# Kernel tuning notes

Measured on AMD Instinct MI355X. Metric: run time of the kernel, lower is better.

Reference implementation:

```python
import jax, jax.numpy as jnp
import numpy as np

B, F, K, DEPTH = 512, 64, 64, 3  # feas == k == 64, deepDepth == 3


def setup_inputs() -> dict:
    key = jax.random.key(0)
    ks = jax.random.split(key, 16)
    x = jax.random.normal(ks[0], (B, F), dtype=jnp.float32)
    # wide: Linear(feas, 1)
    Ww = jax.random.normal(ks[1], (1, F), dtype=jnp.float32) * 0.1
    bw = jnp.zeros((1,), dtype=jnp.float32)
    # cross: Parameter(torch.rand(feas, k))
    cross = jax.random.uniform(ks[2], (F, K), dtype=jnp.float32)
    # attention: Linear(k, k) -> ReLU -> Linear(k, 1, bias=False)
    W1 = jax.random.normal(ks[3], (K, K), dtype=jnp.float32) / np.sqrt(K)
    b1 = jnp.zeros((K,), dtype=jnp.float32)
    w2 = jax.random.normal(ks[4], (K,), dtype=jnp.float32) / np.sqrt(K)
    # deep{i}: Linear(k//i, k//(i+1)) + ReLU, i = 1..DEPTH  -> 64->32->21->16
    dims = [K // i for i in range(1, DEPTH + 2)]  # [64, 32, 21, 16]
    Wd1 = jax.random.normal(ks[5], (dims[1], dims[0]), dtype=jnp.float32) / np.sqrt(dims[0])
    bd1 = jnp.zeros((dims[1],), dtype=jnp.float32)
    Wd2 = jax.random.normal(ks[6], (dims[2], dims[1]), dtype=jnp.float32) / np.sqrt(dims[1])
    bd2 = jnp.zeros((dims[2],), dtype=jnp.float32)
    Wd3 = jax.random.normal(ks[7], (dims[3], dims[2]), dtype=jnp.float32) / np.sqrt(dims[2])
    bd3 = jnp.zeros((dims[3],), dtype=jnp.float32)
    # out: Linear(feas // (deepDepth+1), 1) == Linear(16, 1)
    Wo = jax.random.normal(ks[8], (1, F // (DEPTH + 1)), dtype=jnp.float32) * 0.1
    bo = jnp.zeros((1,), dtype=jnp.float32)
    return {"x": x, "Ww": Ww, "bw": bw, "cross": cross, "W1": W1, "b1": b1,
            "w2": w2, "Wd1": Wd1, "bd1": bd1, "Wd2": Wd2, "bd2": bd2,
            "Wd3": Wd3, "bd3": bd3, "Wo": Wo, "bo": bo}


def reference(x, Ww, bw, cross, W1, b1, w2, Wd1, bd1, Wd2, bd2, Wd3, bd3, Wo, bo):
    linear = x @ Ww.T + bw  # [B, 1]

    # Pairwise FM interactions v[b,i,j,:] = x_i * x_j * (cross_i ∘ cross_j)
    xx = x[:, :, None] * x[:, None, :]                    # [B, F, F]
    cp = cross[:, None, :] * cross[None, :, :]            # [F, F, K]
    v = xx[..., None] * cp[None]                          # [B, F, F, K]

    # attention MLP score per pair
    h = jax.nn.relu(jnp.einsum('bijk,lk->bijl', v, W1) + b1)
    s = jnp.einsum('bijl,l->bij', h, w2)                  # [B, F, F]

    # loop semantics: upper triangle (j >= i), pair kept iff x_i != 0 and x_j != 0
    valid = jnp.triu(jnp.ones((F, F), dtype=bool))[None] \
        & (x[:, :, None] != 0) & (x[:, None, :] != 0)     # [B, F, F]
    neg = jnp.finfo(s.dtype).min
    logits = jnp.where(valid, s, neg)

    # softmax over [0 (seed zeros(1) entry), valid pair scores...];
    # the seed zeros(k) value-vector contributes nothing to the weighted sum.
    m = jnp.maximum(jnp.max(logits, axis=(1, 2)), 0.0)    # [B]
    e = jnp.where(valid, jnp.exp(logits - m[:, None, None]), 0.0)
    denom = jnp.exp(-m) + jnp.sum(e, axis=(1, 2))         # +exp(-m) is the 0-logit term
    tmp = jnp.einsum('bij,bijk->bk', e, v) / denom[:, None]  # [B, K]

    tmp = jax.nn.relu(tmp @ Wd1.T + bd1)
    tmp = jax.nn.relu(tmp @ Wd2.T + bd2)
    tmp = jax.nn.relu(tmp @ Wd3.T + bd3)
    deep_out = tmp @ Wo.T + bo                            # [B, 1]
    return jax.nn.sigmoid(linear + deep_out)
```

## Files before the change

### kernel.cpp

```cpp
#include <hip/hip_runtime.h>
#include <math.h>


#define BB 512
#define FF 64
#define STR 68
#define NPAIRS 2080
#define THREADS 512
#define NEG_BIG -3.402823466e38f

typedef _Float16 half8 __attribute__((ext_vector_type(8)));
typedef _Float16 half4 __attribute__((ext_vector_type(4)));
typedef float f32x4 __attribute__((ext_vector_type(4)));

__device__ __forceinline__ half8 ld8(const _Float16* p) {
    half8 v;
    *(half4*)&v       = *(const half4*)p;
    *((half4*)&v + 1) = *(const half4*)(p + 4);
    return v;
}

__global__ __launch_bounds__(THREADS, 4) void afm_r6_kernel(
    const float* __restrict__ x,
    const float* __restrict__ Ww,
    const float* __restrict__ bw,
    const float* __restrict__ cross,
    const float* __restrict__ W1,
    const float* __restrict__ b1,
    const float* __restrict__ w2,
    const float* __restrict__ Wd1,
    const float* __restrict__ bd1,
    const float* __restrict__ Wd2,
    const float* __restrict__ bd2,
    const float* __restrict__ Wd3,
    const float* __restrict__ bd3,
    const float* __restrict__ Wo,
    const float* __restrict__ bo,
    float* __restrict__ out)
{
    __shared__ __align__(16) _Float16 ah_s [FF * STR];
    __shared__ __align__(16) _Float16 aht_s[FF * STR];
    __shared__ __align__(16) _Float16 M_s  [FF * STR];
    __shared__ float s_s[NPAIRS];
    __shared__ float x_sh[FF];
    __shared__ float part_s[4][FF];
    __shared__ float mlp_s[FF];
    __shared__ float red_s[16];

    const int tid  = threadIdx.x;
    const int lane = tid & 63;
    const int wave = tid >> 6;
    const int b    = blockIdx.x;
    const int m    = lane & 15;
    const int q    = lane >> 4;

    if (tid < FF) x_sh[tid] = x[b * FF + tid];
    __syncthreads();

    for (int idx = tid; idx < FF * FF; idx += THREADS) {
        const int i = idx >> 6, k = idx & 63;
        const _Float16 v = (_Float16)(x_sh[i] * cross[idx]);
        ah_s[i * STR + k]  = v;
        aht_s[k * STR + i] = v;
    }
    for (int idx = tid; idx < (FF * STR) / 2; idx += THREADS)
        ((int*)M_s)[idx] = 0;

    half8 afr[4][2];
    #pragma unroll
    for (int mt = 0; mt < 4; ++mt)
        #pragma unroll
        for (int kt = 0; kt < 2; ++kt) {
            const float* wr = W1 + (mt * 16 + m) * FF + kt * 32 + q * 8;
            half8 h;
            #pragma unroll
            for (int jj = 0; jj < 8; ++jj) h[jj] = (_Float16)wr[jj];
            afr[mt][kt] = h;
        }
    float b1r[16], w2r[16];
    #pragma unroll
    for (int mt = 0; mt < 4; ++mt)
        #pragma unroll
        for (int r = 0; r < 4; ++r) {
            b1r[mt * 4 + r] = b1[mt * 16 + q * 4 + r];
            w2r[mt * 4 + r] = w2[mt * 16 + q * 4 + r];
        }
    __syncthreads();

    #pragma unroll
    for (int g = 0; g < 8; ++g) {
        const int i = wave + 8 * g;
        const int nt = 4 - (g >> 1);
        const int basei = i * FF - (i * (i - 1)) / 2;
        const float xi = x_sh[i];
        const half8 ai0 = ld8(&ah_s[i * STR + q * 8]);
        const half8 ai1 = ld8(&ah_s[i * STR + 32 + q * 8]);
        #pragma unroll
        for (int t = 0; t < nt; ++t) {
            const int j0 = i + 16 * t;
            const int jc = min(j0 + m, 63);
            const half8 bf0 = ai0 * ld8(&ah_s[jc * STR + q * 8]);
            const half8 bf1 = ai1 * ld8(&ah_s[jc * STR + 32 + q * 8]);
            const float xjv = x_sh[jc];
            float sp = 0.f;
            #pragma unroll
            for (int mt = 0; mt < 4; ++mt) {
                f32x4 acc;
                #pragma unroll
                for (int r = 0; r < 4; ++r) acc[r] = b1r[mt * 4 + r];
                acc = __builtin_amdgcn_mfma_f32_16x16x32_f16(afr[mt][0], bf0, acc, 0, 0, 0);
                acc = __builtin_amdgcn_mfma_f32_16x16x32_f16(afr[mt][1], bf1, acc, 0, 0, 0);
                #pragma unroll
                for (int r = 0; r < 4; ++r)
                    sp = fmaf(w2r[mt * 4 + r], fmaxf(acc[r], 0.f), sp);
            }
            sp += __shfl_xor(sp, 16, 64);
            sp += __shfl_xor(sp, 32, 64);
            const bool valid = (xi != 0.f) && (xjv != 0.f);
            if (lane < 16 && (j0 + lane) < FF)
                s_s[basei + 16 * t + lane] = valid ? sp : NEG_BIG;
        }
    }
    __syncthreads();

    float mx = 0.0f;
    for (int p = tid; p < NPAIRS; p += THREADS) mx = fmaxf(mx, s_s[p]);
    #pragma unroll
    for (int off = 32; off > 0; off >>= 1)
        mx = fmaxf(mx, __shfl_xor(mx, off, 64));
    if (lane == 0) red_s[wave] = mx;
    __syncthreads();
    float mval = red_s[0];
    #pragma unroll
    for (int w = 1; w < 8; ++w) mval = fmaxf(mval, red_s[w]);

    float sum = 0.f;
    for (int idx = tid; idx < FF * FF; idx += THREADS) {
        const int i = idx >> 6, j = idx & 63;
        if (j >= i) {
            const int p = i * FF - (i * (i - 1)) / 2 + (j - i);
            const float e = __expf(s_s[p] - mval);
            sum += e;
            M_s[i * STR + j] = (_Float16)e;
        }
    }
    #pragma unroll
    for (int off = 32; off > 0; off >>= 1)
        sum += __shfl_xor(sum, off, 64);
    if (lane == 0) red_s[8 + wave] = sum;
    __syncthreads();
    float denom = __expf(-mval);
    #pragma unroll
    for (int w = 0; w < 8; ++w) denom += red_s[8 + w];

    {
        const int t0 = wave * 2;
        #pragma unroll
        for (int t = t0; t < t0 + 2; ++t) {
            const int i0 = (t >> 2) * 16, k0 = (t & 3) * 16;
            const half8 a0  = ld8(&M_s[(i0 + m) * STR + q * 8]);
            const half8 a1  = ld8(&M_s[(i0 + m) * STR + 32 + q * 8]);
            const half8 bb0 = ld8(&aht_s[(k0 + m) * STR + q * 8]);
            const half8 bb1 = ld8(&aht_s[(k0 + m) * STR + 32 + q * 8]);
            f32x4 gacc = {0.f, 0.f, 0.f, 0.f};
            gacc = __builtin_amdgcn_mfma_f32_16x16x32_f16(a0, bb0, gacc, 0, 0, 0);
            gacc = __builtin_amdgcn_mfma_f32_16x16x32_f16(a1, bb1, gacc, 0, 0, 0);
            const half4 ap = *(const half4*)&aht_s[(k0 + m) * STR + i0 + q * 4];
            float s4 = (float)ap[0] * gacc[0] + (float)ap[1] * gacc[1]
                     + (float)ap[2] * gacc[2] + (float)ap[3] * gacc[3];
            s4 += __shfl_xor(s4, 16, 64);
            s4 += __shfl_xor(s4, 32, 64);
            if (lane < 16) part_s[i0 >> 4][k0 + lane] = s4;
        }
    }
    __syncthreads();
    if (tid < FF)
        mlp_s[tid] = (part_s[0][tid] + part_s[1][tid] +
                      part_s[2][tid] + part_s[3][tid]) / denom;
    __syncthreads();

    float hv = 0.f;
    if (tid < 32) {
        float a1v = bd1[tid];
        for (int k = 0; k < 64; ++k) a1v = fmaf(Wd1[tid * 64 + k], mlp_s[k], a1v);
        hv = fmaxf(a1v, 0.f);
    }
    __syncthreads();
    if (tid < 32) mlp_s[tid] = hv;
    __syncthreads();
    if (tid < 21) {
        float a2 = bd2[tid];
        for (int k = 0; k < 32; ++k) a2 = fmaf(Wd2[tid * 32 + k], mlp_s[k], a2);
        hv = fmaxf(a2, 0.f);
    }
    __syncthreads();
    if (tid < 21) mlp_s[tid] = hv;
    __syncthreads();
    if (tid < 16) {
        float a3 = bd3[tid];
        for (int k = 0; k < 21; ++k) a3 = fmaf(Wd3[tid * 21 + k], mlp_s[k], a3);
        hv = fmaxf(a3, 0.f);
    }
    __syncthreads();
    if (tid < 16) mlp_s[tid] = hv;
    __syncthreads();

    if (tid == 0) {
        float deep = bo[0];
        for (int k = 0; k < 16; ++k) deep = fmaf(Wo[k], mlp_s[k], deep);
        float lin = bw[0];
        for (int k = 0; k < 64; ++k) lin = fmaf(Ww[k], x_sh[k], lin);
        const float z = lin + deep;
        out[b] = 1.f / (1.f + __expf(-z));
    }
}

extern "C" void kernel_launch(void* const* d_in, const int* in_sizes, int n_in,
                              void* d_out, int out_size, void* d_ws, size_t ws_size,
                              hipStream_t stream) {
    const float* xp    = (const float*)d_in[0];
    const float* Ww    = (const float*)d_in[1];
    const float* bw    = (const float*)d_in[2];
    const float* cross = (const float*)d_in[3];
    const float* W1    = (const float*)d_in[4];
    const float* b1    = (const float*)d_in[5];
    const float* w2    = (const float*)d_in[6];
    const float* Wd1   = (const float*)d_in[7];
    const float* bd1   = (const float*)d_in[8];
    const float* Wd2   = (const float*)d_in[9];
    const float* bd2   = (const float*)d_in[10];
    const float* Wd3   = (const float*)d_in[11];
    const float* bd3   = (const float*)d_in[12];
    const float* Wo    = (const float*)d_in[13];
    const float* bo    = (const float*)d_in[14];
    float* outp = (float*)d_out;

    afm_r6_kernel<<<BB, THREADS, 0, stream>>>(xp, Ww, bw, cross, W1, b1, w2,
                                              Wd1, bd1, Wd2, bd2, Wd3, bd3,
                                              Wo, bo, outp);
}
```

Measured before the change: 104.6 us.

## Split AFM kernel into score kernel with two blocks per sample and tail kernel

Splits the fused per-sample kernel in two. The first kernel computes the pairwise attention scores using two blocks per batch row, each taking half of the row indices, and writes them to a global workspace. The second kernel reads the scores back, then runs the softmax, the weighted aggregation and the deep MLP. The aim is to double the number of blocks in the dominant MFMA stage to raise GPU occupancy, at the cost of a second launch, a global round trip for the scores, and duplicated setup work (x*cross staging) in both kernels.

```diff
diff --git a/kernel.cpp b/kernel.cpp
--- a/kernel.cpp
+++ b/kernel.cpp
@@ -20,37 +20,22 @@
     return v;
 }
 
-__global__ __launch_bounds__(THREADS, 4) void afm_r6_kernel(
+__global__ __launch_bounds__(THREADS, 4) void afm_scores_kernel(
     const float* __restrict__ x,
-    const float* __restrict__ Ww,
-    const float* __restrict__ bw,
     const float* __restrict__ cross,
     const float* __restrict__ W1,
     const float* __restrict__ b1,
     const float* __restrict__ w2,
-    const float* __restrict__ Wd1,
-    const float* __restrict__ bd1,
-    const float* __restrict__ Wd2,
-    const float* __restrict__ bd2,
-    const float* __restrict__ Wd3,
-    const float* __restrict__ bd3,
-    const float* __restrict__ Wo,
-    const float* __restrict__ bo,
-    float* __restrict__ out)
+    float* __restrict__ sco)
 {
-    __shared__ __align__(16) _Float16 ah_s [FF * STR];
-    __shared__ __align__(16) _Float16 aht_s[FF * STR];
-    __shared__ __align__(16) _Float16 M_s  [FF * STR];
-    __shared__ float s_s[NPAIRS];
+    __shared__ __align__(16) _Float16 ah_s[FF * STR];
     __shared__ float x_sh[FF];
-    __shared__ float part_s[4][FF];
-    __shared__ float mlp_s[FF];
-    __shared__ float red_s[16];
 
     const int tid  = threadIdx.x;
     const int lane = tid & 63;
     const int wave = tid >> 6;
-    const int b    = blockIdx.x;
+    const int b    = blockIdx.x >> 1;
+    const int h    = blockIdx.x & 1;
     const int m    = lane & 15;
     const int q    = lane >> 4;
 
@@ -59,12 +44,8 @@
 
     for (int idx = tid; idx < FF * FF; idx += THREADS) {
         const int i = idx >> 6, k = idx & 63;
-        const _Float16 v = (_Float16)(x_sh[i] * cross[idx]);
-        ah_s[i * STR + k]  = v;
-        aht_s[k * STR + i] = v;
-    }
-    for (int idx = tid; idx < (FF * STR) / 2; idx += THREADS)
-        ((int*)M_s)[idx] = 0;
+        ah_s[i * STR + k] = (_Float16)(x_sh[i] * cross[idx]);
+    }
 
     half8 afr[4][2];
     #pragma unroll
@@ -72,10 +53,10 @@
         #pragma unroll
         for (int kt = 0; kt < 2; ++kt) {
             const float* wr = W1 + (mt * 16 + m) * FF + kt * 32 + q * 8;
-            half8 h;
+            half8 hh;
             #pragma unroll
-            for (int jj = 0; jj < 8; ++jj) h[jj] = (_Float16)wr[jj];
-            afr[mt][kt] = h;
+            for (int jj = 0; jj < 8; ++jj) hh[jj] = (_Float16)wr[jj];
+            afr[mt][kt] = hh;
         }
     float b1r[16], w2r[16];
     #pragma unroll
@@ -87,10 +68,12 @@
         }
     __syncthreads();
 
-    #pragma unroll
-    for (int g = 0; g < 8; ++g) {
-        const int i = wave + 8 * g;
-        const int nt = 4 - (g >> 1);
+    const int u = h * 8 + wave;
+    float* srow = sco + b * NPAIRS;
+    #pragma unroll
+    for (int g = 0; g < 4; ++g) {
+        const int i = u + 16 * g;
+        const int nt = 4 - g;
         const int basei = i * FF - (i * (i - 1)) / 2;
         const float xi = x_sh[i];
         const half8 ai0 = ld8(&ah_s[i * STR + q * 8]);
@@ -118,13 +101,60 @@
             sp += __shfl_xor(sp, 32, 64);
             const bool valid = (xi != 0.f) && (xjv != 0.f);
             if (lane < 16 && (j0 + lane) < FF)
-                s_s[basei + 16 * t + lane] = valid ? sp : NEG_BIG;
-        }
-    }
-    __syncthreads();
-
+                srow[basei + 16 * t + lane] = valid ? sp : NEG_BIG;
+        }
+    }
+}
+
+__global__ __launch_bounds__(THREADS, 4) void afm_tail_kernel(
+    const float* __restrict__ x,
+    const float* __restrict__ Ww,
+    const float* __restrict__ bw,
+    const float* __restrict__ cross,
+    const float* __restrict__ Wd1,
+    const float* __restrict__ bd1,
+    const float* __restrict__ Wd2,
+    const float* __restrict__ bd2,
+    const float* __restrict__ Wd3,
+    const float* __restrict__ bd3,
+    const float* __restrict__ Wo,
+    const float* __restrict__ bo,
+    const float* __restrict__ sco,
+    float* __restrict__ out)
+{
+    __shared__ __align__(16) _Float16 aht_s[FF * STR];
+    __shared__ __align__(16) _Float16 M_s  [FF * STR];
+    __shared__ float s_s[NPAIRS];
+    __shared__ float x_sh[FF];
+    __shared__ float part_s[4][FF];
+    __shared__ float mlp_s[FF];
+    __shared__ float red_s[16];
+
+    const int tid  = threadIdx.x;
+    const int lane = tid & 63;
+    const int wave = tid >> 6;
+    const int b    = blockIdx.x;
+    const int m    = lane & 15;
+    const int q    = lane >> 4;
+
+    if (tid < FF) x_sh[tid] = x[b * FF + tid];
+    __syncthreads();
+
+    for (int idx = tid; idx < FF * FF; idx += THREADS) {
+        const int i = idx >> 6, k = idx & 63;
+        aht_s[k * STR + i] = (_Float16)(x_sh[i] * cross[idx]);
+    }
+    for (int idx = tid; idx < (FF * STR) / 2; idx += THREADS)
+        ((int*)M_s)[idx] = 0;
+    __syncthreads();
+
+    const float* srow = sco + b * NPAIRS;
     float mx = 0.0f;
-    for (int p = tid; p < NPAIRS; p += THREADS) mx = fmaxf(mx, s_s[p]);
+    for (int p = tid; p < NPAIRS; p += THREADS) {
+        const float v = srow[p];
+        s_s[p] = v;
+        mx = fmaxf(mx, v);
+    }
     #pragma unroll
     for (int off = 32; off > 0; off >>= 1)
         mx = fmaxf(mx, __shfl_xor(mx, off, 64));
@@ -234,8 +264,10 @@
     const float* Wo    = (const float*)d_in[13];
     const float* bo    = (const float*)d_in[14];
     float* outp = (float*)d_out;
-
-    afm_r6_kernel<<<BB, THREADS, 0, stream>>>(xp, Ww, bw, cross, W1, b1, w2,
-                                              Wd1, bd1, Wd2, bd2, Wd3, bd3,
-                                              Wo, bo, outp);
-}
+    float* sco  = (float*)d_ws;
+
+    afm_scores_kernel<<<BB * 2, THREADS, 0, stream>>>(xp, cross, W1, b1, w2, sco);
+    afm_tail_kernel<<<BB, THREADS, 0, stream>>>(xp, Ww, bw, cross,
+                                                Wd1, bd1, Wd2, bd2, Wd3, bd3,
+                                                Wo, bo, sco, outp);
+}
```

Result: slower. 115.1 us (+10.1%).
